# Optimization experiments

Measured on AMD Instinct MI355X. Metric: run time of the kernel, lower is better.

## Reference

```python
import jax, jax.numpy as jnp
import numpy as np

N_NODES = 100000


def _gcn_conv(x, src, dst, W, b, n_nodes):
    # PyG GCNConv: out = D^{-1/2} (A + I) D^{-1/2} (x W) + b
    h = x @ W  # [N, out]
    # degree including self-loop
    ones = jnp.ones(src.shape[0], dtype=h.dtype)
    deg = jax.ops.segment_sum(ones, dst, num_segments=n_nodes) + 1.0
    dinv = jax.lax.rsqrt(deg)  # [N]
    # neighbor messages: gather from src, normalize, scatter-add to dst
    norm = dinv[src] * dinv[dst]  # [E]
    msg = h[src] * norm[:, None]  # [E, out]
    agg = jax.ops.segment_sum(msg, dst, num_segments=n_nodes)
    # self-loop contribution: norm_ii = dinv[i]^2
    agg = agg + h * (dinv * dinv)[:, None]
    return agg + b


def setup_inputs() -> dict:
    key = jax.random.key(0)
    ks = jax.random.split(key, 10)
    x = jax.random.normal(ks[0], (N_NODES, 64), dtype=jnp.float32)
    edge_index = jax.random.randint(ks[1], (2, 1000000), 0, N_NODES, dtype=jnp.int64)
    def glorot(k, shape):
        lim = np.sqrt(6.0 / (shape[0] + shape[1]))
        return jax.random.uniform(k, shape, jnp.float32, -lim, lim)
    return {
        "x": x,
        "edge_index": edge_index,
        "W1": glorot(ks[2], (64, 80)), "b1": jnp.zeros((80,), jnp.float32),
        "W2": glorot(ks[3], (80, 40)), "b2": jnp.zeros((40,), jnp.float32),
        "W3": glorot(ks[4], (40, 50)), "b3": jnp.zeros((50,), jnp.float32),
        "Wl": glorot(ks[5], (50, 10)), "bl": jnp.zeros((10,), jnp.float32),
    }


def reference(x, edge_index, W1, b1, W2, b2, W3, b3, Wl, bl):
    src, dst = edge_index[0], edge_index[1]
    n = x.shape[0]
    h = _gcn_conv(x, src, dst, W1, b1, n)
    h = jax.nn.leaky_relu(h, negative_slope=0.01)
    # dropout is identity in eval mode
    h = _gcn_conv(h, src, dst, W2, b2, n)
    h = jax.nn.leaky_relu(h, negative_slope=0.01)
    h = _gcn_conv(h, src, dst, W3, b3, n)
    h = jax.nn.leaky_relu(h, negative_slope=0.01)
    logits = h @ Wl + bl
    return jax.nn.log_softmax(logits, axis=1)
```

## Files before the change

### kernel.cpp

```cpp
#include <hip/hip_runtime.h>

#define LEAKY(v) ((v) > 0.0f ? (v) : 0.01f * (v))
#define NBUK_MAX 512

typedef __attribute__((ext_vector_type(8))) short bf16x8;
typedef __attribute__((ext_vector_type(4))) float f32x4;

__device__ __forceinline__ unsigned short f2bf(float f) {
    unsigned u = __float_as_uint(f);
    u += 0x7fffu + ((u >> 16) & 1u);
    return (unsigned short)(u >> 16);
}
__device__ __forceinline__ unsigned pack2bf(float lo, float hi) {
    return (unsigned)f2bf(lo) | ((unsigned)f2bf(hi) << 16);
}
__device__ __forceinline__ float4 bf4_to_f4(uint2 u) {
    float4 r;
    r.x = __uint_as_float(u.x << 16);
    r.y = __uint_as_float(u.x & 0xffff0000u);
    r.z = __uint_as_float(u.y << 16);
    r.w = __uint_as_float(u.y & 0xffff0000u);
    return r;
}

__device__ __forceinline__ int detect_is64(const unsigned* ei, int E) {
    __shared__ int is64_s;
    if (threadIdx.x == 0) {
        int z = 1;
        int limit = 2 * E < 128 ? 2 * E : 128;
        for (int i = 1; i < limit; i += 2)
            if (ei[i] != 0u) { z = 0; break; }
        is64_s = z;
    }
    __syncthreads();
    return is64_s;
}

__global__ __launch_bounds__(256) void bucket_count_kernel(
    const unsigned* __restrict__ ei, int* __restrict__ s32, int* __restrict__ d32,
    int* __restrict__ gcount, int E, int nblk, int nbuk, int ch) {
    __shared__ int hist[NBUK_MAX];
    int is64 = detect_is64(ei, E);
    for (int i = threadIdx.x; i < nbuk; i += 256) hist[i] = 0;
    __syncthreads();
    int base = blockIdx.x * ch;
    int lim = min(base + ch, E);
    for (int e = base + threadIdx.x; e < lim; e += 256) {
        int s, d;
        if (is64) {
            s = (int)ei[2 * (size_t)e];
            d = (int)ei[2 * (size_t)E + 2 * (size_t)e];
        } else {
            s = (int)ei[e];
            d = (int)ei[(size_t)E + e];
        }
        s32[e] = s;
        d32[e] = d;
        atomicAdd(&hist[d >> 8], 1);
    }
    __syncthreads();
    for (int i = threadIdx.x; i < nbuk; i += 256)
        gcount[(size_t)i * nblk + blockIdx.x] = hist[i];
}

__global__ __launch_bounds__(256) void bucket_total_kernel(
    const int* __restrict__ gcount, int* __restrict__ btot, int nblk) {
    __shared__ int s[256];
    int sum = 0;
    for (int i = threadIdx.x; i < nblk; i += 256)
        sum += gcount[(size_t)blockIdx.x * nblk + i];
    s[threadIdx.x] = sum;
    __syncthreads();
    for (int off = 128; off > 0; off >>= 1) {
        if (threadIdx.x < off) s[threadIdx.x] += s[threadIdx.x + off];
        __syncthreads();
    }
    if (threadIdx.x == 0) btot[blockIdx.x] = s[0];
}

__global__ __launch_bounds__(512) void scan_btot_kernel(
    const int* __restrict__ btot, int* __restrict__ bbase,
    int* __restrict__ row_ofs, int nbuk, int N, int E) {
    __shared__ int s[512];
    int t = threadIdx.x;
    int v = (t < nbuk) ? btot[t] : 0;
    s[t] = v;
    __syncthreads();
    for (int off = 1; off < 512; off <<= 1) {
        int add = (t >= off) ? s[t - off] : 0;
        __syncthreads();
        s[t] += add;
        __syncthreads();
    }
    if (t < nbuk) bbase[t] = s[t] - v;
    if (t == 0) { bbase[nbuk] = E; row_ofs[N] = E; }
}

__global__ __launch_bounds__(256) void scan_gcount_kernel(
    int* __restrict__ gcount, const int* __restrict__ bbase, int nblk) {
    __shared__ int s[256];
    int t = threadIdx.x;
    int v = (t < nblk) ? gcount[(size_t)blockIdx.x * nblk + t] : 0;
    s[t] = v;
    __syncthreads();
    for (int off = 1; off < 256; off <<= 1) {
        int add = (t >= off) ? s[t - off] : 0;
        __syncthreads();
        s[t] += add;
        __syncthreads();
    }
    if (t < nblk)
        gcount[(size_t)blockIdx.x * nblk + t] = bbase[blockIdx.x] + s[t] - v;
}

__global__ __launch_bounds__(256) void bucket_scatter_kernel(
    const int* __restrict__ s32, const int* __restrict__ d32,
    const int* __restrict__ gofs, unsigned* __restrict__ es_tmp,
    int E, int nblk, int nbuk, int ch) {
    __shared__ int cur[NBUK_MAX];
    for (int i = threadIdx.x; i < nbuk; i += 256)
        cur[i] = gofs[(size_t)i * nblk + blockIdx.x];
    __syncthreads();
    int base = blockIdx.x * ch;
    int lim = min(base + ch, E);
    for (int e = base + threadIdx.x; e < lim; e += 256) {
        int s = s32[e], d = d32[e];
        int p = atomicAdd(&cur[d >> 8], 1);
        es_tmp[p] = ((unsigned)(d & 255) << 24) | (unsigned)s;
    }
}

__global__ __launch_bounds__(256) void bucket_sortcvt_kernel(
    const unsigned* __restrict__ es_tmp, const int* __restrict__ bbase,
    int* __restrict__ es, int* __restrict__ row_ofs, float* __restrict__ dinv,
    const float* __restrict__ x, ushort4* __restrict__ xb, int N) {
    __shared__ int hist[256];
    __shared__ int lofs[256];
    __shared__ float sdinv[256];
    int b = blockIdx.x;
    int t = threadIdx.x;
    int beg = bbase[b], end = bbase[b + 1];
    hist[t] = 0;
    __syncthreads();
    for (int j = beg + t; j < end; j += 256)
        atomicAdd(&hist[es_tmp[j] >> 24], 1);
    __syncthreads();
    int v = hist[t];
    lofs[t] = v;
    __syncthreads();
    for (int off = 1; off < 256; off <<= 1) {
        int add = (t >= off) ? lofs[t - off] : 0;
        __syncthreads();
        lofs[t] += add;
        __syncthreads();
    }
    int excl = lofs[t] - v;
    int node = (b << 8) + t;
    float dv = rsqrtf((float)v + 1.0f);
    if (node <= N) row_ofs[node] = beg + excl;
    if (node < N) dinv[node] = dv;
    sdinv[t] = dv;
    __syncthreads();
    lofs[t] = beg + excl;
    __syncthreads();
    for (int j = beg + t; j < end; j += 256) {
        unsigned ed = es_tmp[j];
        int p = atomicAdd(&lofs[ed >> 24], 1);
        es[p] = (int)(ed & 0xFFFFFFu);
    }
    int qbase = (b << 8) * 16;
    for (int q = t; q < 256 * 16; q += 256) {
        int nl = q >> 4;
        int n = (b << 8) + nl;
        if (n >= N) break;
        float dn = sdinv[nl];
        float4 vv = ((const float4*)x)[qbase + q];
        ushort4 o;
        o.x = f2bf(vv.x * dn); o.y = f2bf(vv.y * dn);
        o.z = f2bf(vv.z * dn); o.w = f2bf(vv.w * dn);
        xb[qbase + q] = o;
    }
}

__global__ __launch_bounds__(256) void prep_wfrags_kernel(
    const float* __restrict__ W1, const float* __restrict__ W2,
    unsigned short* __restrict__ wfrag) {
    int t = blockIdx.x * 256 + threadIdx.x;
    if (t >= 2432) return;
    const float* W;
    int u, NKC, M, K;
    if (t < 1280) { u = t; W = W1; NKC = 2; M = 80; K = 64; }
    else          { u = t - 1280; W = W2; NKC = 3; M = 40; K = 80; }
    int f = u >> 6, lane = u & 63;
    int s = f & 1, mtkc = f >> 1;
    int kc = mtkc % NKC, mt = mtkc / NKC;
    int col = mt * 16 + (lane & 15);
#pragma unroll
    for (int j = 0; j < 8; ++j) {
        int k = kc * 32 + ((lane >> 4) << 3) + j;
        float w = (k < K && col < M) ? W[k * M + col] : 0.0f;
        unsigned short hi = f2bf(w);
        unsigned short v = s ? f2bf(w - __uint_as_float((unsigned)hi << 16)) : hi;
        wfrag[(size_t)t * 8 + j] = v;
    }
}

__global__ __launch_bounds__(256) void l1l2_fused_kernel(
    const unsigned short* __restrict__ xb, const int* __restrict__ es,
    const int* __restrict__ row_ofs, const float* __restrict__ dinv,
    const unsigned short* __restrict__ wfrag, const float* __restrict__ b1,
    unsigned short* __restrict__ Pb, int N) {
    constexpr int NFR = 38;
    __shared__ bf16x8 wlds[NFR * 64];
    __shared__ unsigned short atile[4][16 * 88];
    for (int i = threadIdx.x; i < NFR * 64; i += 256) {
        int f = i >> 6, ln = i & 63;
        wlds[f * 64 + (ln ^ (ln >> 3))] = *(const bf16x8*)&wfrag[(size_t)i * 8];
    }
    __syncthreads();
    int wid = blockIdx.x * 4 + (threadIdx.x >> 6);
    int ntiles = (N + 15) >> 4;
    if (wid >= ntiles) return;
    int lane = threadIdx.x & 63;
    int row = lane & 15, kid = lane >> 4;
    int lidx = lane ^ (lane >> 3);
    int base = wid * 16;
    int node = base + row;
    bool act = node < N;
    int beg = 0, end = 0;
    float dd = 0.f;
    if (act) {
        beg = row_ofs[node];
        end = row_ofs[node + 1];
        dd = dinv[node];
    }
    const char* xbb = (const char*)xb;
    const int o0 = kid * 16;
    const int o1 = 64 + kid * 16;
    float4 aL0 = make_float4(0.f, 0.f, 0.f, 0.f);
    float4 aL1 = make_float4(0.f, 0.f, 0.f, 0.f);
    float4 aH0 = make_float4(0.f, 0.f, 0.f, 0.f);
    float4 aH1 = make_float4(0.f, 0.f, 0.f, 0.f);
#define ACCU(u, c0, c1)                                             \
    {                                                               \
        float4 lo_ = bf4_to_f4(make_uint2((u).x, (u).y));           \
        float4 hi_ = bf4_to_f4(make_uint2((u).z, (u).w));           \
        c0.x += lo_.x; c0.y += lo_.y; c0.z += lo_.z; c0.w += lo_.w; \
        c1.x += hi_.x; c1.y += hi_.y; c1.z += hi_.z; c1.w += hi_.w; \
    }
    int j = beg;
    for (; j + 4 <= end; j += 4) {
        int s0 = es[j], s1 = es[j + 1], s2 = es[j + 2], s3 = es[j + 3];
        const char* p0 = xbb + (size_t)s0 * 128;
        const char* p1 = xbb + (size_t)s1 * 128;
        const char* p2 = xbb + (size_t)s2 * 128;
        const char* p3 = xbb + (size_t)s3 * 128;
        uint4 u00 = *(const uint4*)(p0 + o0);
        uint4 u01 = *(const uint4*)(p0 + o1);
        uint4 u10 = *(const uint4*)(p1 + o0);
        uint4 u11 = *(const uint4*)(p1 + o1);
        uint4 u20 = *(const uint4*)(p2 + o0);
        uint4 u21 = *(const uint4*)(p2 + o1);
        uint4 u30 = *(const uint4*)(p3 + o0);
        uint4 u31 = *(const uint4*)(p3 + o1);
        ACCU(u00, aL0, aL1) ACCU(u01, aH0, aH1)
        ACCU(u10, aL0, aL1) ACCU(u11, aH0, aH1)
        ACCU(u20, aL0, aL1) ACCU(u21, aH0, aH1)
        ACCU(u30, aL0, aL1) ACCU(u31, aH0, aH1)
    }
    for (; j < end; ++j) {
        int s0 = es[j];
        const char* p0 = xbb + (size_t)s0 * 128;
        uint4 u00 = *(const uint4*)(p0 + o0);
        uint4 u01 = *(const uint4*)(p0 + o1);
        ACCU(u00, aL0, aL1) ACCU(u01, aH0, aH1)
    }
    if (act) {
        const char* ps = xbb + (size_t)node * 128;
        uint4 us0 = *(const uint4*)(ps + o0);
        uint4 us1 = *(const uint4*)(ps + o1);
        ACCU(us0, aL0, aL1) ACCU(us1, aH0, aH1)
    }
#undef ACCU
    bf16x8 a0, a1;
    a0[0] = (short)f2bf(aL0.x * dd); a0[1] = (short)f2bf(aL0.y * dd);
    a0[2] = (short)f2bf(aL0.z * dd); a0[3] = (short)f2bf(aL0.w * dd);
    a0[4] = (short)f2bf(aL1.x * dd); a0[5] = (short)f2bf(aL1.y * dd);
    a0[6] = (short)f2bf(aL1.z * dd); a0[7] = (short)f2bf(aL1.w * dd);
    a1[0] = (short)f2bf(aH0.x * dd); a1[1] = (short)f2bf(aH0.y * dd);
    a1[2] = (short)f2bf(aH0.z * dd); a1[3] = (short)f2bf(aH0.w * dd);
    a1[4] = (short)f2bf(aH1.x * dd); a1[5] = (short)f2bf(aH1.y * dd);
    a1[6] = (short)f2bf(aH1.z * dd); a1[7] = (short)f2bf(aH1.w * dd);

    f32x4 acc[5];
#pragma unroll
    for (int mt = 0; mt < 5; ++mt) acc[mt] = (f32x4){0.f, 0.f, 0.f, 0.f};
#pragma unroll
    for (int mt = 0; mt < 5; ++mt) {
        acc[mt] = __builtin_amdgcn_mfma_f32_16x16x32_bf16(
            a0, wlds[((mt * 2 + 0) * 2 + 0) * 64 + lidx], acc[mt], 0, 0, 0);
        acc[mt] = __builtin_amdgcn_mfma_f32_16x16x32_bf16(
            a0, wlds[((mt * 2 + 0) * 2 + 1) * 64 + lidx], acc[mt], 0, 0, 0);
        acc[mt] = __builtin_amdgcn_mfma_f32_16x16x32_bf16(
            a1, wlds[((mt * 2 + 1) * 2 + 0) * 64 + lidx], acc[mt], 0, 0, 0);
        acc[mt] = __builtin_amdgcn_mfma_f32_16x16x32_bf16(
            a1, wlds[((mt * 2 + 1) * 2 + 1) * 64 + lidx], acc[mt], 0, 0, 0);
    }
    unsigned short* at = atile[threadIdx.x >> 6];
#pragma unroll
    for (int mt = 0; mt < 5; ++mt) {
        int col = mt * 16 + (lane & 15);
        float bb = b1[col];
#pragma unroll
        for (int r = 0; r < 4; ++r) {
            float v = acc[mt][r] + bb;
            v = LEAKY(v);
            at[(kid * 4 + r) * 88 + col] = f2bf(v);
        }
    }
    bf16x8 a2[3];
#pragma unroll
    for (int kc = 0; kc < 3; ++kc) {
        int k0 = kc * 32 + kid * 8;
        if (k0 + 8 <= 80)
            a2[kc] = *(const bf16x8*)&at[(lane & 15) * 88 + k0];
        else
            a2[kc] = (bf16x8){0, 0, 0, 0, 0, 0, 0, 0};
    }
    f32x4 acc2[3];
#pragma unroll
    for (int mt = 0; mt < 3; ++mt) acc2[mt] = (f32x4){0.f, 0.f, 0.f, 0.f};
#pragma unroll
    for (int mt = 0; mt < 3; ++mt) {
#pragma unroll
        for (int kc = 0; kc < 3; ++kc) {
            acc2[mt] = __builtin_amdgcn_mfma_f32_16x16x32_bf16(
                a2[kc], wlds[(20 + (mt * 3 + kc) * 2 + 0) * 64 + lidx], acc2[mt], 0, 0, 0);
            acc2[mt] = __builtin_amdgcn_mfma_f32_16x16x32_bf16(
                a2[kc], wlds[(20 + (mt * 3 + kc) * 2 + 1) * 64 + lidx], acc2[mt], 0, 0, 0);
        }
    }
    float dvr[4];
#pragma unroll
    for (int r = 0; r < 4; ++r)
        dvr[r] = dinv[min(base + kid * 4 + r, N - 1)];
#pragma unroll
    for (int mt = 0; mt < 3; ++mt) {
        int col = mt * 16 + (lane & 15);
        if (col >= 40) continue;
#pragma unroll
        for (int r = 0; r < 4; ++r) {
            int orow = base + kid * 4 + r;
            if (orow < N)
                Pb[(size_t)orow * 40 + col] = f2bf(acc2[mt][r] * dvr[r]);
        }
    }
}

template <bool BIAS, bool PRESCALE_LEAKY>
__global__ __launch_bounds__(256) void gather40_bf16_kernel(
    const unsigned short* __restrict__ hb, const int* __restrict__ es,
    const int* __restrict__ row_ofs, const float* __restrict__ dinv,
    const float* __restrict__ b, unsigned short* __restrict__ agg, int N) {
    int wid = (blockIdx.x * blockDim.x + threadIdx.x) >> 6;
    int lane = threadIdx.x & 63;
    int g = lane / 5;
    int l = lane - g * 5;
    int node = wid * 12 + g;
    bool active = (g < 12) && (node < N);
    int beg = 0, end = 0;
    float dd = 0.f;
    if (active) {
        beg = row_ofs[node];
        end = row_ofs[node + 1];
        dd = dinv[node];
    }
    float4 aL = make_float4(0.f, 0.f, 0.f, 0.f);
    float4 aH = make_float4(0.f, 0.f, 0.f, 0.f);
#define ACC40(u)                                                    \
    {                                                               \
        float4 lo_ = bf4_to_f4(make_uint2((u).x, (u).y));           \
        float4 hi_ = bf4_to_f4(make_uint2((u).z, (u).w));           \
        aL.x += lo_.x; aL.y += lo_.y; aL.z += lo_.z; aL.w += lo_.w; \
        aH.x += hi_.x; aH.y += hi_.y; aH.z += hi_.z; aH.w += hi_.w; \
    }
    int j = beg;
    for (; j + 4 <= end; j += 4) {
        int s0 = es[j], s1 = es[j + 1], s2 = es[j + 2], s3 = es[j + 3];
        uint4 h0 = *(const uint4*)&hb[(size_t)s0 * 40 + 8 * l];
        uint4 h1 = *(const uint4*)&hb[(size_t)s1 * 40 + 8 * l];
        uint4 h2 = *(const uint4*)&hb[(size_t)s2 * 40 + 8 * l];
        uint4 h3 = *(const uint4*)&hb[(size_t)s3 * 40 + 8 * l];
        ACC40(h0) ACC40(h1) ACC40(h2) ACC40(h3)
    }
    for (; j < end; ++j) {
        int s0 = es[j];
        uint4 h0 = *(const uint4*)&hb[(size_t)s0 * 40 + 8 * l];
        ACC40(h0)
    }
#undef ACC40
    if (active) {
        uint4 sr = *(const uint4*)&hb[(size_t)node * 40 + 8 * l];
        float4 sL = bf4_to_f4(make_uint2(sr.x, sr.y));
        float4 sH = bf4_to_f4(make_uint2(sr.z, sr.w));
        float r0 = (aL.x + sL.x) * dd, r1 = (aL.y + sL.y) * dd;
        float r2 = (aL.z + sL.z) * dd, r3 = (aL.w + sL.w) * dd;
        float r4 = (aH.x + sH.x) * dd, r5 = (aH.y + sH.y) * dd;
        float r6 = (aH.z + sH.z) * dd, r7 = (aH.w + sH.w) * dd;
        if (BIAS) {
            float4 b0 = *(const float4*)&b[8 * l];
            float4 b1 = *(const float4*)&b[8 * l + 4];
            r0 += b0.x; r1 += b0.y; r2 += b0.z; r3 += b0.w;
            r4 += b1.x; r5 += b1.y; r6 += b1.z; r7 += b1.w;
        }
        if (PRESCALE_LEAKY) {
            r0 = LEAKY(r0) * dd; r1 = LEAKY(r1) * dd;
            r2 = LEAKY(r2) * dd; r3 = LEAKY(r3) * dd;
            r4 = LEAKY(r4) * dd; r5 = LEAKY(r5) * dd;
            r6 = LEAKY(r6) * dd; r7 = LEAKY(r7) * dd;
        }
        uint4 o;
        o.x = pack2bf(r0, r1); o.y = pack2bf(r2, r3);
        o.z = pack2bf(r4, r5); o.w = pack2bf(r6, r7);
        *(uint4*)&agg[(size_t)node * 40 + 8 * l] = o;
    }
}

__global__ __launch_bounds__(256) void l3head_kernel(
    const unsigned short* __restrict__ P, const float* __restrict__ W3,
    const float* __restrict__ b3, const float* __restrict__ Wl,
    const float* __restrict__ bl, float* __restrict__ out, int N) {
    __shared__ float w3s[40 * 50];
    __shared__ float b3s[50];
    __shared__ float wls[50 * 10];
    __shared__ float bls[10];
    for (int i = threadIdx.x; i < 2000; i += 256) w3s[i] = W3[i];
    for (int i = threadIdx.x; i < 500; i += 256) wls[i] = Wl[i];
    if (threadIdx.x < 50) b3s[threadIdx.x] = b3[threadIdx.x];
    if (threadIdx.x < 10) bls[threadIdx.x] = bl[threadIdx.x];
    __syncthreads();
    int n = blockIdx.x * blockDim.x + threadIdx.x;
    if (n >= N) return;

    float p[40];
    const uint2* pr = (const uint2*)(P + (size_t)n * 40);
#pragma unroll
    for (int q = 0; q < 10; ++q) {
        float4 t = bf4_to_f4(pr[q]);
        p[4 * q + 0] = t.x; p[4 * q + 1] = t.y; p[4 * q + 2] = t.z; p[4 * q + 3] = t.w;
    }
    float logits[10];
#pragma unroll
    for (int j = 0; j < 10; ++j) logits[j] = bls[j];
    for (int m = 0; m < 50; ++m) {
        float acc = b3s[m];
#pragma unroll
        for (int k = 0; k < 40; ++k) acc = fmaf(p[k], w3s[k * 50 + m], acc);
        float v = LEAKY(acc);
#pragma unroll
        for (int j = 0; j < 10; ++j) logits[j] = fmaf(v, wls[m * 10 + j], logits[j]);
    }
    float mx = logits[0];
#pragma unroll
    for (int j = 1; j < 10; ++j) mx = fmaxf(mx, logits[j]);
    float s = 0.0f;
#pragma unroll
    for (int j = 0; j < 10; ++j) s += __expf(logits[j] - mx);
    float lse = __logf(s) + mx;
    float* op = out + (size_t)n * 10;
#pragma unroll
    for (int j = 0; j < 10; ++j) op[j] = logits[j] - lse;
}

extern "C" void kernel_launch(void* const* d_in, const int* in_sizes, int n_in,
                              void* d_out, int out_size, void* d_ws, size_t ws_size,
                              hipStream_t stream) {
    const float* x  = (const float*)d_in[0];
    const unsigned* ei = (const unsigned*)d_in[1];
    const float* W1 = (const float*)d_in[2];
    const float* b1 = (const float*)d_in[3];
    const float* W2 = (const float*)d_in[4];
    const float* b2 = (const float*)d_in[5];
    const float* W3 = (const float*)d_in[6];
    const float* b3 = (const float*)d_in[7];
    const float* Wl = (const float*)d_in[8];
    const float* bl = (const float*)d_in[9];
    float* out = (float*)d_out;

    const int N = in_sizes[0] / 64;
    const int E = in_sizes[1] / 2;

    int ch = 4096;
    int nblk = (E + ch - 1) / ch;
    if (nblk > 256) { ch = (E + 255) / 256; nblk = (E + ch - 1) / ch; }
    const int nbuk = (N + 255) >> 8;

    char* wp = (char*)d_ws;
    auto alloc = [&](size_t bytes) {
        char* p = wp;
        wp += (bytes + 255) & ~(size_t)255;
        return p;
    };
    int*   es      = (int*)alloc((size_t)E * 4);
    float* dinv    = (float*)alloc((size_t)N * 4);
    int*   row_ofs = (int*)alloc((size_t)(N + 1) * 4);
    int*   gcount  = (int*)alloc((size_t)nbuk * nblk * 4);
    int*   btot    = (int*)alloc((size_t)NBUK_MAX * 4);
    int*   bbase   = (int*)alloc((size_t)(NBUK_MAX + 1) * 4);
    unsigned short* wfrag = (unsigned short*)alloc((size_t)2432 * 8 * 2);
    char*  Pr      = (char*)alloc((size_t)N * 64 * 4);
    char*  Ar      = (char*)alloc((size_t)N * 80 * 4);

    int*      s32    = (int*)Pr;
    int*      d32    = (int*)Pr + E;
    unsigned* es_tmp = (unsigned*)Ar;
    size_t xb_off = (((size_t)E * 4) + 255) & ~(size_t)255;
    unsigned short* xb = (unsigned short*)(Ar + xb_off);
    unsigned short* Pb = (unsigned short*)Pr;
    unsigned short* Ab = (unsigned short*)(Ar + (size_t)N * 80 * 4 - (size_t)N * 40 * 2);
    unsigned short* P3 = (unsigned short*)Pr;

    const int B = 256;

    prep_wfrags_kernel<<<10, B, 0, stream>>>(W1, W2, wfrag);

    bucket_count_kernel<<<nblk, B, 0, stream>>>(ei, s32, d32, gcount, E, nblk, nbuk, ch);
    bucket_total_kernel<<<nbuk, B, 0, stream>>>(gcount, btot, nblk);
    scan_btot_kernel<<<1, 512, 0, stream>>>(btot, bbase, row_ofs, nbuk, N, E);
    scan_gcount_kernel<<<nbuk, B, 0, stream>>>(gcount, bbase, nblk);
    bucket_scatter_kernel<<<nblk, B, 0, stream>>>(s32, d32, gcount, es_tmp, E, nblk, nbuk, ch);
    bucket_sortcvt_kernel<<<nbuk, B, 0, stream>>>(es_tmp, bbase, es, row_ofs, dinv,
                                                  x, (ushort4*)xb, N);

    const int blk40 = ((N + 11) / 12 + 3) / 4;
    const int ntiles = (N + 15) / 16;
    const int gemm_blocks = (ntiles + 3) / 4;

    l1l2_fused_kernel<<<gemm_blocks, B, 0, stream>>>(xb, es, row_ofs, dinv, wfrag, b1, Pb, N);

    gather40_bf16_kernel<true, true><<<blk40, B, 0, stream>>>(Pb, es, row_ofs, dinv, b2, Ab, N);

    gather40_bf16_kernel<false, false><<<blk40, B, 0, stream>>>(Ab, es, row_ofs, dinv, nullptr, P3, N);
    l3head_kernel<<<(N + B - 1) / B, B, 0, stream>>>(P3, W3, b3, Wl, bl, out, N);
}
```

Baseline: 257.1 us.

## Split layer-1 gather from MFMA GEMM into column-sliced gather kernel

The fused layer-1 kernel that gathered 64-wide bf16 neighbor rows and then ran the MFMA GEMM is split into two kernels. The new gather kernel uses one thread per node and one of 8 column slices per block, so neighbor loads are spread over more blocks. The GEMM kernel then reads the aggregated rows from an intermediate buffer, and the buffer roles are rearranged to make room for it. This adds an extra write and read of an N×64 bf16 intermediate plus a launch, in exchange for more gather parallelism and a leaner GEMM kernel.

```diff
diff --git a/kernel.cpp b/kernel.cpp
--- a/kernel.cpp
+++ b/kernel.cpp
@@ -205,9 +205,56 @@
     }
 }
 
-__global__ __launch_bounds__(256) void l1l2_fused_kernel(
+__global__ __launch_bounds__(256) void gather64_sliced_kernel(
     const unsigned short* __restrict__ xb, const int* __restrict__ es,
     const int* __restrict__ row_ofs, const float* __restrict__ dinv,
+    unsigned short* __restrict__ Pg, int N) {
+    int tile = blockIdx.x >> 3;
+    int c = blockIdx.x & 7;
+    int node = tile * 256 + threadIdx.x;
+    if (node >= N) return;
+    int beg = row_ofs[node], end = row_ofs[node + 1];
+    float dd = dinv[node];
+    const char* xbb = (const char*)xb;
+    const int oc = c * 16;
+    float4 aL = make_float4(0.f, 0.f, 0.f, 0.f);
+    float4 aH = make_float4(0.f, 0.f, 0.f, 0.f);
+#define ACCS(u)                                                     \
+    {                                                               \
+        float4 lo_ = bf4_to_f4(make_uint2((u).x, (u).y));           \
+        float4 hi_ = bf4_to_f4(make_uint2((u).z, (u).w));           \
+        aL.x += lo_.x; aL.y += lo_.y; aL.z += lo_.z; aL.w += lo_.w; \
+        aH.x += hi_.x; aH.y += hi_.y; aH.z += hi_.z; aH.w += hi_.w; \
+    }
+    int j = beg;
+    for (; j + 4 <= end; j += 4) {
+        int s0 = es[j], s1 = es[j + 1], s2 = es[j + 2], s3 = es[j + 3];
+        uint4 u0 = *(const uint4*)(xbb + (size_t)s0 * 128 + oc);
+        uint4 u1 = *(const uint4*)(xbb + (size_t)s1 * 128 + oc);
+        uint4 u2 = *(const uint4*)(xbb + (size_t)s2 * 128 + oc);
+        uint4 u3 = *(const uint4*)(xbb + (size_t)s3 * 128 + oc);
+        ACCS(u0) ACCS(u1) ACCS(u2) ACCS(u3)
+    }
+    for (; j < end; ++j) {
+        int s0 = es[j];
+        uint4 u0 = *(const uint4*)(xbb + (size_t)s0 * 128 + oc);
+        ACCS(u0)
+    }
+    {
+        uint4 us = *(const uint4*)(xbb + (size_t)node * 128 + oc);
+        ACCS(us)
+    }
+#undef ACCS
+    uint4 o;
+    o.x = pack2bf(aL.x * dd, aL.y * dd);
+    o.y = pack2bf(aL.z * dd, aL.w * dd);
+    o.z = pack2bf(aH.x * dd, aH.y * dd);
+    o.w = pack2bf(aH.z * dd, aH.w * dd);
+    *(uint4*)&Pg[(size_t)node * 64 + c * 8] = o;
+}
+
+__global__ __launch_bounds__(256) void gemm12_fused_kernel(
+    const unsigned short* __restrict__ Pg, const float* __restrict__ dinv,
     const unsigned short* __restrict__ wfrag, const float* __restrict__ b1,
     unsigned short* __restrict__ Pb, int N) {
     constexpr int NFR = 38;
@@ -222,75 +269,14 @@
     int ntiles = (N + 15) >> 4;
     if (wid >= ntiles) return;
     int lane = threadIdx.x & 63;
-    int row = lane & 15, kid = lane >> 4;
+    int kid = lane >> 4;
     int lidx = lane ^ (lane >> 3);
     int base = wid * 16;
-    int node = base + row;
-    bool act = node < N;
-    int beg = 0, end = 0;
-    float dd = 0.f;
-    if (act) {
-        beg = row_ofs[node];
-        end = row_ofs[node + 1];
-        dd = dinv[node];
-    }
-    const char* xbb = (const char*)xb;
-    const int o0 = kid * 16;
-    const int o1 = 64 + kid * 16;
-    float4 aL0 = make_float4(0.f, 0.f, 0.f, 0.f);
-    float4 aL1 = make_float4(0.f, 0.f, 0.f, 0.f);
-    float4 aH0 = make_float4(0.f, 0.f, 0.f, 0.f);
-    float4 aH1 = make_float4(0.f, 0.f, 0.f, 0.f);
-#define ACCU(u, c0, c1)                                             \
-    {                                                               \
-        float4 lo_ = bf4_to_f4(make_uint2((u).x, (u).y));           \
-        float4 hi_ = bf4_to_f4(make_uint2((u).z, (u).w));           \
-        c0.x += lo_.x; c0.y += lo_.y; c0.z += lo_.z; c0.w += lo_.w; \
-        c1.x += hi_.x; c1.y += hi_.y; c1.z += hi_.z; c1.w += hi_.w; \
-    }
-    int j = beg;
-    for (; j + 4 <= end; j += 4) {
-        int s0 = es[j], s1 = es[j + 1], s2 = es[j + 2], s3 = es[j + 3];
-        const char* p0 = xbb + (size_t)s0 * 128;
-        const char* p1 = xbb + (size_t)s1 * 128;
-        const char* p2 = xbb + (size_t)s2 * 128;
-        const char* p3 = xbb + (size_t)s3 * 128;
-        uint4 u00 = *(const uint4*)(p0 + o0);
-        uint4 u01 = *(const uint4*)(p0 + o1);
-        uint4 u10 = *(const uint4*)(p1 + o0);
-        uint4 u11 = *(const uint4*)(p1 + o1);
-        uint4 u20 = *(const uint4*)(p2 + o0);
-        uint4 u21 = *(const uint4*)(p2 + o1);
-        uint4 u30 = *(const uint4*)(p3 + o0);
-        uint4 u31 = *(const uint4*)(p3 + o1);
-        ACCU(u00, aL0, aL1) ACCU(u01, aH0, aH1)
-        ACCU(u10, aL0, aL1) ACCU(u11, aH0, aH1)
-        ACCU(u20, aL0, aL1) ACCU(u21, aH0, aH1)
-        ACCU(u30, aL0, aL1) ACCU(u31, aH0, aH1)
-    }
-    for (; j < end; ++j) {
-        int s0 = es[j];
-        const char* p0 = xbb + (size_t)s0 * 128;
-        uint4 u00 = *(const uint4*)(p0 + o0);
-        uint4 u01 = *(const uint4*)(p0 + o1);
-        ACCU(u00, aL0, aL1) ACCU(u01, aH0, aH1)
-    }
-    if (act) {
-        const char* ps = xbb + (size_t)node * 128;
-        uint4 us0 = *(const uint4*)(ps + o0);
-        uint4 us1 = *(const uint4*)(ps + o1);
-        ACCU(us0, aL0, aL1) ACCU(us1, aH0, aH1)
-    }
-#undef ACCU
-    bf16x8 a0, a1;
-    a0[0] = (short)f2bf(aL0.x * dd); a0[1] = (short)f2bf(aL0.y * dd);
-    a0[2] = (short)f2bf(aL0.z * dd); a0[3] = (short)f2bf(aL0.w * dd);
-    a0[4] = (short)f2bf(aL1.x * dd); a0[5] = (short)f2bf(aL1.y * dd);
-    a0[6] = (short)f2bf(aL1.z * dd); a0[7] = (short)f2bf(aL1.w * dd);
-    a1[0] = (short)f2bf(aH0.x * dd); a1[1] = (short)f2bf(aH0.y * dd);
-    a1[2] = (short)f2bf(aH0.z * dd); a1[3] = (short)f2bf(aH0.w * dd);
-    a1[4] = (short)f2bf(aH1.x * dd); a1[5] = (short)f2bf(aH1.y * dd);
-    a1[6] = (short)f2bf(aH1.z * dd); a1[7] = (short)f2bf(aH1.w * dd);
+    int arow = base + (lane & 15);
+    if (arow >= N) arow = N - 1;
+
+    bf16x8 a0 = *(const bf16x8*)&Pg[(size_t)arow * 64 + kid * 8];
+    bf16x8 a1 = *(const bf16x8*)&Pg[(size_t)arow * 64 + 32 + kid * 8];
 
     f32x4 acc[5];
 #pragma unroll
@@ -516,9 +502,10 @@
     unsigned* es_tmp = (unsigned*)Ar;
     size_t xb_off = (((size_t)E * 4) + 255) & ~(size_t)255;
     unsigned short* xb = (unsigned short*)(Ar + xb_off);
-    unsigned short* Pb = (unsigned short*)Pr;
-    unsigned short* Ab = (unsigned short*)(Ar + (size_t)N * 80 * 4 - (size_t)N * 40 * 2);
-    unsigned short* P3 = (unsigned short*)Pr;
+    unsigned short* Pg = (unsigned short*)Pr;
+    unsigned short* Pb = (unsigned short*)Ar;
+    unsigned short* Ab = (unsigned short*)Pr;
+    unsigned short* P3 = (unsigned short*)Ar;
 
     const int B = 256;
 
@@ -535,8 +522,10 @@
     const int blk40 = ((N + 11) / 12 + 3) / 4;
     const int ntiles = (N + 15) / 16;
     const int gemm_blocks = (ntiles + 3) / 4;
-
-    l1l2_fused_kernel<<<gemm_blocks, B, 0, stream>>>(xb, es, row_ofs, dinv, wfrag, b1, Pb, N);
+    const int tile256 = (N + 255) / 256;
+
+    gather64_sliced_kernel<<<tile256 * 8, B, 0, stream>>>(xb, es, row_ofs, dinv, Pg, N);
+    gemm12_fused_kernel<<<gemm_blocks, B, 0, stream>>>(Pg, dinv, wfrag, b1, Pb, N);
 
     gather40_bf16_kernel<true, true><<<blk40, B, 0, stream>>>(Pb, es, row_ofs, dinv, b2, Ab, N);
 
```

Result: slower. 374.0 us (+45.5%).
